# Kernel optimization log

Hardware: AMD Instinct MI355X
Metric: run time of the kernel (lower is better)

Reference implementation:

```python
import jax, jax.numpy as jnp
import numpy as np

MAX_RADIUS = 0.9
TEMP = 0.1

def _to_poincare(x, W, b):
    # Linear + Tanh, then rescale into Poincare ball of radius 0.9
    h = jnp.tanh(x @ W.T + b)
    norm = jnp.clip(jnp.linalg.norm(h, axis=-1, keepdims=True), 1e-8, None)
    scale = jnp.where(norm > MAX_RADIUS, MAX_RADIUS / norm, jnp.ones_like(norm))
    return h * scale

def setup_inputs() -> dict:
    key = jax.random.key(0)
    kq, kw, kb, km, ko = jax.random.split(key, 5)
    B, N, D = 2048, 100000, 128
    return {
        "query": jax.random.normal(kq, (B, D), dtype=jnp.float32),
        "W": jax.random.normal(kw, (D, D), dtype=jnp.float32) * (1.0 / np.sqrt(D)),
        "b": jax.random.normal(kb, (D,), dtype=jnp.float32) * 0.01,
        "mem_emb": jax.random.normal(km, (N, D), dtype=jnp.float32),
        "mem_out": jax.random.normal(ko, (N, D), dtype=jnp.float32),
        "k": 16,
    }

def reference(query, W, b, mem_emb, mem_out, k):
    q = _to_poincare(query, W, b)          # [B, D]
    m = _to_poincare(mem_emb, W, b)        # [N, D]
    # Euclidean cdist via the GEMM form: ||q||^2 + ||m||^2 - 2 q.m
    q2 = jnp.sum(q * q, axis=-1, keepdims=True)           # [B, 1]
    m2 = jnp.sum(m * m, axis=-1)                          # [N]
    d2 = q2 + m2[None, :] - 2.0 * (q @ m.T)               # [B, N]
    dists = jnp.sqrt(jnp.maximum(d2, 1e-12))
    # k smallest distances
    neg_top, top_idx = jax.lax.top_k(-dists, k)           # [B, k]
    top_dists = -neg_top
    weights = jax.nn.softmax(-top_dists / TEMP, axis=-1)  # [B, k]
    outcomes = mem_out[top_idx]                           # [B, k, D]
    return weights, outcomes
```

## Files before the change

### kernel.cpp

```cpp
#include <hip/hip_runtime.h>
#include <hip/hip_bf16.h>
#include <math.h>

#define DIM 128
#define QB 64
#define MB 64
#define NSPLIT 32
#define KSEL 16
#define KOWN 4
#define RESCORE 32
#define IDXMASK 0x1FFFu
#define KEYMASK 0xFFFFE000u

using bf16x8 = __attribute__((ext_vector_type(8))) short;
using f32x4  = __attribute__((ext_vector_type(4))) float;

__device__ inline unsigned short f2bf(float f) {
  __hip_bfloat16 h = __float2bfloat16(f);
  return __builtin_bit_cast(unsigned short, h);
}

__device__ inline f32x4 mfma16(bf16x8 a, bf16x8 b, f32x4 c) {
  return __builtin_amdgcn_mfma_f32_16x16x32_bf16(a, b, c, 0, 0, 0);
}

__device__ inline void gload_lds16(const void* g, void* l) {
  __builtin_amdgcn_global_load_lds(
      (const __attribute__((address_space(1))) void*)g,
      (__attribute__((address_space(3))) void*)l, 16, 0, 0);
}

__global__ __launch_bounds__(512) void poincare2_k(
    const float* __restrict__ Xm, int Rm,
    const float* __restrict__ Xq, int Rq,
    const float* __restrict__ W, const float* __restrict__ bias,
    float* __restrict__ Pm, float* __restrict__ Pm2,
    unsigned short* __restrict__ Pmbf,
    float* __restrict__ Pq, float* __restrict__ Pq2, int nbm)
{
  __shared__ float Wl[DIM * DIM];
  __shared__ float nrm[128 * 17];
  __shared__ float norm2l[128];

  const int t  = threadIdx.x;
  const int cg = t & 15;
  const int rg = t >> 4;

  const bool ismem = (int)blockIdx.x < nbm;
  const float* X = ismem ? Xm : Xq;
  const int    R = ismem ? Rm : Rq;
  float*       P  = ismem ? Pm  : Pq;
  float*       P2 = ismem ? Pm2 : Pq2;
  unsigned short* Pbf = ismem ? Pmbf : nullptr;
  const int rbase = (ismem ? blockIdx.x : (blockIdx.x - nbm)) * 128;

  for (int i = t; i < DIM * 32; i += 512) {
    const int j = i >> 5, c = i & 31;
    const float4 v = *(const float4*)&W[j * DIM + c * 4];
    *(float4*)&Wl[j * DIM + ((c ^ ((j >> 3) & 7)) << 2)] = v;
  }
  float bj[8];
  #pragma unroll
  for (int u = 0; u < 8; ++u) bj[u] = bias[cg * 8 + u];

  const float* xr[4];
  #pragma unroll
  for (int v = 0; v < 4; ++v) {
    int row = rbase + rg + 32 * v;
    if (row > R - 1) row = R - 1;
    xr[v] = X + (size_t)row * DIM;
  }
  __syncthreads();

  float acc[4][8];
  #pragma unroll
  for (int v = 0; v < 4; ++v)
    #pragma unroll
    for (int u = 0; u < 8; ++u) acc[v][u] = bj[u];

  #pragma unroll 2
  for (int k4 = 0; k4 < 32; ++k4) {
    float4 xv[4], wv[8];
    #pragma unroll
    for (int v = 0; v < 4; ++v) xv[v] = *(const float4*)&xr[v][k4 * 4];
    #pragma unroll
    for (int u = 0; u < 8; ++u) {
      const int j = cg * 8 + u;
      wv[u] = *(const float4*)&Wl[j * DIM + ((k4 ^ ((j >> 3) & 7)) << 2)];
    }
    #pragma unroll
    for (int v = 0; v < 4; ++v)
      #pragma unroll
      for (int u = 0; u < 8; ++u) {
        acc[v][u] = fmaf(xv[v].x, wv[u].x, acc[v][u]);
        acc[v][u] = fmaf(xv[v].y, wv[u].y, acc[v][u]);
        acc[v][u] = fmaf(xv[v].z, wv[u].z, acc[v][u]);
        acc[v][u] = fmaf(xv[v].w, wv[u].w, acc[v][u]);
      }
  }

  #pragma unroll
  for (int v = 0; v < 4; ++v) {
    float pn = 0.f;
    #pragma unroll
    for (int u = 0; u < 8; ++u) {
      const float th = tanhf(acc[v][u]);
      acc[v][u] = th;
      pn = fmaf(th, th, pn);
    }
    nrm[(rg + 32 * v) * 17 + cg] = pn;
  }
  __syncthreads();
  if (t < 128) {
    float s = 0.f;
    #pragma unroll
    for (int c2 = 0; c2 < 16; ++c2) s += nrm[t * 17 + c2];
    norm2l[t] = s;
    if (rbase + t < R) {
      const float nm = sqrtf(s);
      const float sc = (nm > 0.9f) ? (0.9f / nm) : 1.0f;
      P2[rbase + t] = s * sc * sc;
    }
  }
  __syncthreads();

  #pragma unroll
  for (int v = 0; v < 4; ++v) {
    const int r = rg + 32 * v;
    const int row = rbase + r;
    if (row < R) {
      const float n2 = norm2l[r];
      const float nm = sqrtf(n2);
      const float sc = (nm > 0.9f) ? (0.9f / nm) : 1.0f;
      float o[8];
      #pragma unroll
      for (int u = 0; u < 8; ++u) o[u] = acc[v][u] * sc;
      *(float4*)&P[(size_t)row * DIM + cg * 8]     = make_float4(o[0], o[1], o[2], o[3]);
      *(float4*)&P[(size_t)row * DIM + cg * 8 + 4] = make_float4(o[4], o[5], o[6], o[7]);
      if (Pbf) {
        uint4 pb;
        pb.x = (unsigned)f2bf(o[0]) | ((unsigned)f2bf(o[1]) << 16);
        pb.y = (unsigned)f2bf(o[2]) | ((unsigned)f2bf(o[3]) << 16);
        pb.z = (unsigned)f2bf(o[4]) | ((unsigned)f2bf(o[5]) << 16);
        pb.w = (unsigned)f2bf(o[6]) | ((unsigned)f2bf(o[7]) << 16);
        *(uint4*)&Pmbf[(size_t)row * DIM + ((cg ^ (row & 7)) << 3)] = pb;
      }
    }
  }
}

template<bool USEBF>
__global__ __launch_bounds__(512, 8) void score_topk_k(
    const float* __restrict__ Pq,
    const float* __restrict__ Pm, const float* __restrict__ Pm2,
    const unsigned short* __restrict__ Pmbf,
    int N, int splitlen, unsigned* __restrict__ splitTop)
{
  __shared__ __align__(16) unsigned short Ml0[MB * DIM];
  __shared__ __align__(16) unsigned short Ml1[MB * DIM];
  __shared__ float m20[MB], m21[MB];

  const int t = threadIdx.x;
  const int lane = t & 63;
  const int w = t >> 6, wr = w >> 1, wc = w & 1;
  const int split = blockIdx.x;
  const int qbase = blockIdx.y * QB;
  const int mlo = split * splitlen;
  const int mhi = min(mlo + splitlen, N);

  bf16x8 qf[4];
  {
    const int qrow = qbase + wr * 16 + (lane & 15);
    #pragma unroll
    for (int ks = 0; ks < 4; ++ks) {
      const float* src = &Pq[(size_t)qrow * DIM + ks * 32 + (lane >> 4) * 8];
      float4 lo = *(const float4*)src;
      float4 hi = *(const float4*)(src + 4);
      bf16x8 v;
      v[0] = (short)f2bf(lo.x); v[1] = (short)f2bf(lo.y);
      v[2] = (short)f2bf(lo.z); v[3] = (short)f2bf(lo.w);
      v[4] = (short)f2bf(hi.x); v[5] = (short)f2bf(hi.y);
      v[6] = (short)f2bf(hi.z); v[7] = (short)f2bf(hi.w);
      qf[ks] = v;
    }
  }

  const size_t soff0 = (size_t)(w * 8 + (lane >> 4)) * DIM + ((lane & 15) << 3);
  const size_t soff1 = soff0 + 4 * DIM;
  unsigned short* const d00 = &Ml0[(w * 8) * DIM];
  unsigned short* const d01 = &Ml0[(w * 8 + 4) * DIM];
  unsigned short* const d10 = &Ml1[(w * 8) * DIM];
  unsigned short* const d11 = &Ml1[(w * 8 + 4) * DIM];

  auto stage = [&](int mbase, unsigned short* dA, unsigned short* dB,
                   unsigned short* lds) {
    if constexpr (USEBF) {
      const unsigned short* b = Pmbf + (size_t)mbase * DIM;
      gload_lds16(b + soff0, dA);
      gload_lds16(b + soff1, dB);
    } else {
      const int fr = t >> 3, fe = t & 7;
      const float* src = Pm + (size_t)(mbase + fr) * DIM + fe * 16;
      float4 a0 = *(const float4*)(src + 0);
      float4 a1 = *(const float4*)(src + 4);
      float4 a2 = *(const float4*)(src + 8);
      float4 a3 = *(const float4*)(src + 12);
      uint4 o0, o1;
      o0.x = (unsigned)f2bf(a0.x) | ((unsigned)f2bf(a0.y) << 16);
      o0.y = (unsigned)f2bf(a0.z) | ((unsigned)f2bf(a0.w) << 16);
      o0.z = (unsigned)f2bf(a1.x) | ((unsigned)f2bf(a1.y) << 16);
      o0.w = (unsigned)f2bf(a1.z) | ((unsigned)f2bf(a1.w) << 16);
      o1.x = (unsigned)f2bf(a2.x) | ((unsigned)f2bf(a2.y) << 16);
      o1.y = (unsigned)f2bf(a2.z) | ((unsigned)f2bf(a2.w) << 16);
      o1.z = (unsigned)f2bf(a3.x) | ((unsigned)f2bf(a3.y) << 16);
      o1.w = (unsigned)f2bf(a3.z) | ((unsigned)f2bf(a3.w) << 16);
      char* base = (char*)lds + fr * 256;
      *(uint4*)(base + (((2 * fe)     ^ (fr & 7)) << 4)) = o0;
      *(uint4*)(base + (((2 * fe + 1) ^ (fr & 7)) << 4)) = o1;
    }
  };

  const int ntiles = (mhi - mlo + MB - 1) / MB;
  const int mcol = wc * 32 + (lane & 15);

  stage(mlo, d00, d01, Ml0);
  if (t < MB) {
    const int gr = mlo + t;
    m20[t] = (gr < mhi) ? (Pm2[gr] + 2.0f) : __int_as_float(0x7f800000);
  }
  __syncthreads();

  unsigned keys[4][KOWN];
  #pragma unroll
  for (int r = 0; r < 4; ++r)
    #pragma unroll
    for (int i = 0; i < KOWN; ++i) keys[r][i] = 0xFFFFFFFFu;

  auto body = [&](int tile, const unsigned short* ldsCur,
                  unsigned short* dA, unsigned short* dB, unsigned short* ldsNxt,
                  const float* m2cur, float* m2nxt) {
    const int mbase = mlo + tile * MB;
    const bool more = (tile + 1 < ntiles);
    if (more) {
      stage(mbase + MB, dA, dB, ldsNxt);
      if (t < MB) {
        const int gr = mbase + MB + t;
        m2nxt[t] = (gr < mhi) ? (Pm2[gr] + 2.0f) : __int_as_float(0x7f800000);
      }
    }

    const float m2a = m2cur[mcol];
    const float m2b = m2cur[mcol + 16];

    f32x4 acc0 = (f32x4){0.f, 0.f, 0.f, 0.f};
    f32x4 acc1 = (f32x4){0.f, 0.f, 0.f, 0.f};

    const int rowA = mcol;
    const int rowB = mcol + 16;
    __builtin_amdgcn_s_setprio(1);
    #pragma unroll
    for (int ks = 0; ks < 4; ++ks) {
      const int kb = ks * 64 + (lane >> 4) * 16;
      bf16x8 bfrA = *(const bf16x8*)((const char*)ldsCur + rowA * 256 +
                                     (kb ^ ((rowA & 7) << 4)));
      bf16x8 bfrB = *(const bf16x8*)((const char*)ldsCur + rowB * 256 +
                                     (kb ^ ((rowB & 7) << 4)));
      acc0 = mfma16(qf[ks], bfrA, acc0);
      acc1 = mfma16(qf[ks], bfrB, acc1);
    }
    __builtin_amdgcn_s_setprio(0);

    const unsigned idx0 = (unsigned)(tile * MB + mcol);
    #pragma unroll
    for (int r = 0; r < 4; ++r) {
      {
        const float d2 = fmaf(-2.0f, acc0[r], m2a);
        unsigned c = (__float_as_uint(d2) & KEYMASK) | idx0;
        #pragma unroll
        for (int i = 0; i < KOWN; ++i) {
          const unsigned lo = c < keys[r][i] ? c : keys[r][i];
          c = c < keys[r][i] ? keys[r][i] : c;
          keys[r][i] = lo;
        }
      }
      {
        const float d2 = fmaf(-2.0f, acc1[r], m2b);
        unsigned c = (__float_as_uint(d2) & KEYMASK) | (idx0 + 16);
        #pragma unroll
        for (int i = 0; i < KOWN; ++i) {
          const unsigned lo = c < keys[r][i] ? c : keys[r][i];
          c = c < keys[r][i] ? keys[r][i] : c;
          keys[r][i] = lo;
        }
      }
    }
    __syncthreads();
  };

  int tile = 0;
  while (true) {
    body(tile, Ml0, d10, d11, Ml1, m20, m21); if (++tile == ntiles) break;
    body(tile, Ml1, d00, d01, Ml0, m21, m20); if (++tile == ntiles) break;
  }

  #pragma unroll
  for (int r = 0; r < 4; ++r) {
    unsigned k0 = keys[r][0], k1 = keys[r][1];
    unsigned k2 = keys[r][2], k3 = keys[r][3];
    unsigned out = 0xFFFFFFFFu;
    for (int round = 0; round < 8; ++round) {
      unsigned g = k0, o;
      o = __shfl_xor(g, 1, 16); g = o < g ? o : g;
      o = __shfl_xor(g, 2, 16); g = o < g ? o : g;
      o = __shfl_xor(g, 4, 16); g = o < g ? o : g;
      o = __shfl_xor(g, 8, 16); g = o < g ? o : g;
      const bool mine = (k0 == g);
      k0 = mine ? k1 : k0;
      k1 = mine ? k2 : k1;
      k2 = mine ? k3 : k2;
      k3 = mine ? 0xFFFFFFFFu : k3;
      if ((lane & 15) == round) out = g;
    }
    const int q = qbase + wr * 16 + (lane >> 4) * 4 + r;
    if ((lane & 15) < 8)
      splitTop[(((size_t)q * NSPLIT + split) * 2 + wc) * 8 + (lane & 15)] = out;
  }
}

__global__ __launch_bounds__(256) void finalize_k(
    const unsigned* __restrict__ splitTop,
    const float* __restrict__ Pq, const float* __restrict__ Pq2,
    const float* __restrict__ Pm, const float* __restrict__ Pm2,
    const float* __restrict__ memOut, int N, int splitlen,
    float* __restrict__ outW, float* __restrict__ outO)
{
  const int q = blockIdx.x;
  const int t = threadIdx.x;
  __shared__ unsigned selKey[RESCORE];
  __shared__ int      selSrc[RESCORE];
  __shared__ unsigned long long keyx[RESCORE];
  __shared__ unsigned long long selB[KSEL];
  __shared__ float el[KSEL];

  if (t < 64) {
    const unsigned* gp = splitTop + (size_t)q * (NSPLIT * 2 * 8) + t * 8;
    unsigned a[8];
    #pragma unroll
    for (int i = 0; i < 8; ++i) a[i] = gp[i];
    for (int r = 0; r < RESCORE; ++r) {
      unsigned g = a[0], o;
      #pragma unroll
      for (int st = 1; st < 64; st <<= 1) { o = __shfl_xor(g, st); g = o < g ? o : g; }
      unsigned long long mask = __ballot(a[0] == g);
      const int fl = __ffsll((unsigned long long)mask) - 1;
      if (t == fl) {
        selKey[r] = g;
        selSrc[r] = t;
        #pragma unroll
        for (int i = 0; i < 7; ++i) a[i] = a[i + 1];
        a[7] = 0xFFFFFFFFu;
      }
    }
  }
  __syncthreads();

  {
    const int g = t >> 3, e = t & 7;
    const int gidx = (selSrc[g] >> 1) * splitlen + (int)(selKey[g] & IDXMASK);
    const float4* qr = (const float4*)&Pq[(size_t)q * DIM];
    const float4* mr = (const float4*)&Pm[(size_t)gidx * DIM];
    float s = 0.f;
    #pragma unroll
    for (int u = 0; u < 4; ++u) {
      float4 a = qr[e * 4 + u], b = mr[e * 4 + u];
      s = fmaf(a.x, b.x, s); s = fmaf(a.y, b.y, s);
      s = fmaf(a.z, b.z, s); s = fmaf(a.w, b.w, s);
    }
    s += __shfl_xor(s, 1, 8);
    s += __shfl_xor(s, 2, 8);
    s += __shfl_xor(s, 4, 8);
    if (e == 0) {
      float d2 = (Pq2[q] + Pm2[gidx]) - 2.0f * s;
      float dist = sqrtf(fmaxf(d2, 1e-12f));
      keyx[g] = (((unsigned long long)__float_as_uint(dist)) << 32) | (unsigned)gidx;
    }
  }
  __syncthreads();

  if (t < 64) {
    unsigned long long kk = (t < RESCORE) ? keyx[t] : ~0ull;
    for (int r = 0; r < KSEL; ++r) {
      unsigned long long g = kk;
      #pragma unroll
      for (int o = 1; o < 64; o <<= 1) {
        unsigned long long s = __shfl_xor(g, o);
        g = (s < g) ? s : g;
      }
      if (kk == g) kk = ~0ull;
      if (t == 0) selB[r] = g;
    }
  }
  __syncthreads();

  if (t < KSEL) {
    const float d  = __uint_as_float((unsigned)(selB[t] >> 32));
    const float d0 = __uint_as_float((unsigned)(selB[0] >> 32));
    el[t] = expf(-(d / 0.1f) + (d0 / 0.1f));
  }
  __syncthreads();
  if (t < KSEL) {
    float sum = 0.f;
    #pragma unroll
    for (int i = 0; i < KSEL; ++i) sum += el[i];
    outW[(size_t)q * KSEL + t] = el[t] / sum;
  }

  for (int f4 = t; f4 < KSEL * 32; f4 += 256) {
    int r = f4 >> 5, c4 = f4 & 31;
    int idx = (int)(selB[r] & 0xffffffffu);
    *(float4*)&outO[((size_t)q * KSEL + r) * DIM + c4 * 4] =
        *(const float4*)&memOut[(size_t)idx * DIM + c4 * 4];
  }
}

extern "C" void kernel_launch(void* const* d_in, const int* in_sizes, int n_in,
                              void* d_out, int out_size, void* d_ws, size_t ws_size,
                              hipStream_t stream)
{
  const float* query   = (const float*)d_in[0];
  const float* W       = (const float*)d_in[1];
  const float* bias    = (const float*)d_in[2];
  const float* mem_emb = (const float*)d_in[3];
  const float* mem_out = (const float*)d_in[4];
  const int B = in_sizes[0] / DIM;
  const int N = in_sizes[3] / DIM;
  const int N_pad = ((N + MB + 15) / 16) * 16;

  const int splitlen = ((N + NSPLIT * MB - 1) / (NSPLIT * MB)) * MB;

  float* ws  = (float*)d_ws;
  float* Pm  = ws;
  float* Pm2 = Pm + (size_t)N_pad * DIM;
  float* Pq  = Pm2 + N_pad;
  float* Pq2 = Pq + (size_t)B * DIM;
  unsigned* splitTop = (unsigned*)(Pq2 + B);
  unsigned short* Pmbf = (unsigned short*)(splitTop + (size_t)B * NSPLIT * 2 * 8);
  const size_t need_bf = (size_t)((char*)(Pmbf + (size_t)N_pad * DIM) - (char*)d_ws);
  const bool usebf = ws_size >= need_bf;

  float* outW = (float*)d_out;
  float* outO = outW + (size_t)B * KSEL;

  const int nbm = (N + 127) / 128;
  const int nbq = (B + 127) / 128;
  poincare2_k<<<dim3(nbm + nbq), dim3(512), 0, stream>>>(
      mem_emb, N, query, B, W, bias, Pm, Pm2, usebf ? Pmbf : nullptr, Pq, Pq2, nbm);

  dim3 grid2(NSPLIT, B / QB);
  if (usebf)
    score_topk_k<true><<<grid2, dim3(512), 0, stream>>>(Pq, Pm, Pm2, Pmbf, N,
                                                        splitlen, splitTop);
  else
    score_topk_k<false><<<grid2, dim3(512), 0, stream>>>(Pq, Pm, Pm2, nullptr, N,
                                                         splitlen, splitTop);

  finalize_k<<<dim3(B), dim3(256), 0, stream>>>(splitTop, Pq, Pq2, Pm, Pm2,
                                                mem_out, N, splitlen, outW, outO);
}
```

Measured before the change: 222.7 us.

## Fold distance offset into MFMA accumulator init and make finalize one query per wave

The query fragments are negated and the per-row m2 term is pre-scaled to 0.5*m2+1, so the MFMA accumulator starts at that bias and the score key comes straight from the accumulator without a separate fma. Compare-select pairs become explicit unsigned min/max builtins. The finalize kernel now handles four queries per block, one per wavefront, and drops all block-wide barriers in favour of per-wave shared arrays. This trades some rescaling of the key value, which keeps the same ordering, for fewer VALU ops in the hot scoring loop and less sync overhead in finalize.

```diff
diff --git a/kernel.cpp b/kernel.cpp
--- a/kernel.cpp
+++ b/kernel.cpp
@@ -18,6 +18,16 @@
 __device__ inline unsigned short f2bf(float f) {
   __hip_bfloat16 h = __float2bfloat16(f);
   return __builtin_bit_cast(unsigned short, h);
+}
+__device__ inline unsigned uminu(unsigned a, unsigned b) {
+  return __builtin_elementwise_min(a, b);
+}
+__device__ inline unsigned umaxu(unsigned a, unsigned b) {
+  return __builtin_elementwise_max(a, b);
+}
+__device__ inline unsigned long long umin64(unsigned long long a,
+                                            unsigned long long b) {
+  return __builtin_elementwise_min(a, b);
 }
 
 __device__ inline f32x4 mfma16(bf16x8 a, bf16x8 b, f32x4 c) {
@@ -177,10 +187,10 @@
       float4 lo = *(const float4*)src;
       float4 hi = *(const float4*)(src + 4);
       bf16x8 v;
-      v[0] = (short)f2bf(lo.x); v[1] = (short)f2bf(lo.y);
-      v[2] = (short)f2bf(lo.z); v[3] = (short)f2bf(lo.w);
-      v[4] = (short)f2bf(hi.x); v[5] = (short)f2bf(hi.y);
-      v[6] = (short)f2bf(hi.z); v[7] = (short)f2bf(hi.w);
+      v[0] = (short)f2bf(-lo.x); v[1] = (short)f2bf(-lo.y);
+      v[2] = (short)f2bf(-lo.z); v[3] = (short)f2bf(-lo.w);
+      v[4] = (short)f2bf(-hi.x); v[5] = (short)f2bf(-hi.y);
+      v[6] = (short)f2bf(-hi.z); v[7] = (short)f2bf(-hi.w);
       qf[ks] = v;
     }
   }
@@ -226,7 +236,8 @@
   stage(mlo, d00, d01, Ml0);
   if (t < MB) {
     const int gr = mlo + t;
-    m20[t] = (gr < mhi) ? (Pm2[gr] + 2.0f) : __int_as_float(0x7f800000);
+    m20[t] = (gr < mhi) ? fmaf(0.5f, Pm2[gr], 1.0f)
+                        : __int_as_float(0x7f800000);
   }
   __syncthreads();
 
@@ -245,15 +256,16 @@
       stage(mbase + MB, dA, dB, ldsNxt);
       if (t < MB) {
         const int gr = mbase + MB + t;
-        m2nxt[t] = (gr < mhi) ? (Pm2[gr] + 2.0f) : __int_as_float(0x7f800000);
-      }
-    }
-
-    const float m2a = m2cur[mcol];
-    const float m2b = m2cur[mcol + 16];
-
-    f32x4 acc0 = (f32x4){0.f, 0.f, 0.f, 0.f};
-    f32x4 acc1 = (f32x4){0.f, 0.f, 0.f, 0.f};
+        m2nxt[t] = (gr < mhi) ? fmaf(0.5f, Pm2[gr], 1.0f)
+                              : __int_as_float(0x7f800000);
+      }
+    }
+
+    const float ca = m2cur[mcol];
+    const float cb = m2cur[mcol + 16];
+
+    f32x4 acc0 = (f32x4){ca, ca, ca, ca};
+    f32x4 acc1 = (f32x4){cb, cb, cb, cb};
 
     const int rowA = mcol;
     const int rowB = mcol + 16;
@@ -274,22 +286,20 @@
     #pragma unroll
     for (int r = 0; r < 4; ++r) {
       {
-        const float d2 = fmaf(-2.0f, acc0[r], m2a);
-        unsigned c = (__float_as_uint(d2) & KEYMASK) | idx0;
+        unsigned c = (__float_as_uint(acc0[r]) & KEYMASK) | idx0;
         #pragma unroll
         for (int i = 0; i < KOWN; ++i) {
-          const unsigned lo = c < keys[r][i] ? c : keys[r][i];
-          c = c < keys[r][i] ? keys[r][i] : c;
+          const unsigned lo = uminu(c, keys[r][i]);
+          c = umaxu(c, keys[r][i]);
           keys[r][i] = lo;
         }
       }
       {
-        const float d2 = fmaf(-2.0f, acc1[r], m2b);
-        unsigned c = (__float_as_uint(d2) & KEYMASK) | (idx0 + 16);
+        unsigned c = (__float_as_uint(acc1[r]) & KEYMASK) | (idx0 + 16);
         #pragma unroll
         for (int i = 0; i < KOWN; ++i) {
-          const unsigned lo = c < keys[r][i] ? c : keys[r][i];
-          c = c < keys[r][i] ? keys[r][i] : c;
+          const unsigned lo = uminu(c, keys[r][i]);
+          c = umaxu(c, keys[r][i]);
           keys[r][i] = lo;
         }
       }
@@ -309,11 +319,11 @@
     unsigned k2 = keys[r][2], k3 = keys[r][3];
     unsigned out = 0xFFFFFFFFu;
     for (int round = 0; round < 8; ++round) {
-      unsigned g = k0, o;
-      o = __shfl_xor(g, 1, 16); g = o < g ? o : g;
-      o = __shfl_xor(g, 2, 16); g = o < g ? o : g;
-      o = __shfl_xor(g, 4, 16); g = o < g ? o : g;
-      o = __shfl_xor(g, 8, 16); g = o < g ? o : g;
+      unsigned g = k0;
+      g = uminu(g, __shfl_xor(g, 1, 16));
+      g = uminu(g, __shfl_xor(g, 2, 16));
+      g = uminu(g, __shfl_xor(g, 4, 16));
+      g = uminu(g, __shfl_xor(g, 8, 16));
       const bool mine = (k0 == g);
       k0 = mine ? k1 : k0;
       k1 = mine ? k2 : k1;
@@ -334,39 +344,47 @@
     const float* __restrict__ memOut, int N, int splitlen,
     float* __restrict__ outW, float* __restrict__ outO)
 {
-  const int q = blockIdx.x;
-  const int t = threadIdx.x;
-  __shared__ unsigned selKey[RESCORE];
-  __shared__ int      selSrc[RESCORE];
-  __shared__ unsigned long long keyx[RESCORE];
-  __shared__ unsigned long long selB[KSEL];
-  __shared__ float el[KSEL];
-
-  if (t < 64) {
-    const unsigned* gp = splitTop + (size_t)q * (NSPLIT * 2 * 8) + t * 8;
+  const int wv   = threadIdx.x >> 6;
+  const int lane = threadIdx.x & 63;
+  const int q = blockIdx.x * 4 + wv;
+
+  __shared__ unsigned      sKey[4][RESCORE];
+  __shared__ unsigned char sSrc[4][RESCORE];
+  __shared__ unsigned long long sKeyx[4][RESCORE];
+  __shared__ unsigned long long sSel[4][KSEL];
+  __shared__ float sEl[4][KSEL];
+
+  {
+    const unsigned* gp = splitTop + (size_t)q * (NSPLIT * 2 * 8) + lane * 8;
     unsigned a[8];
-    #pragma unroll
-    for (int i = 0; i < 8; ++i) a[i] = gp[i];
+    uint4 lo = *(const uint4*)gp;
+    uint4 hi = *(const uint4*)(gp + 4);
+    a[0] = lo.x; a[1] = lo.y; a[2] = lo.z; a[3] = lo.w;
+    a[4] = hi.x; a[5] = hi.y; a[6] = hi.z; a[7] = hi.w;
     for (int r = 0; r < RESCORE; ++r) {
-      unsigned g = a[0], o;
-      #pragma unroll
-      for (int st = 1; st < 64; st <<= 1) { o = __shfl_xor(g, st); g = o < g ? o : g; }
+      unsigned g = a[0];
+      g = uminu(g, __shfl_xor(g, 1));
+      g = uminu(g, __shfl_xor(g, 2));
+      g = uminu(g, __shfl_xor(g, 4));
+      g = uminu(g, __shfl_xor(g, 8));
+      g = uminu(g, __shfl_xor(g, 16));
+      g = uminu(g, __shfl_xor(g, 32));
       unsigned long long mask = __ballot(a[0] == g);
       const int fl = __ffsll((unsigned long long)mask) - 1;
-      if (t == fl) {
-        selKey[r] = g;
-        selSrc[r] = t;
+      if (lane == fl) {
         #pragma unroll
         for (int i = 0; i < 7; ++i) a[i] = a[i + 1];
         a[7] = 0xFFFFFFFFu;
       }
-    }
-  }
-  __syncthreads();
-
-  {
-    const int g = t >> 3, e = t & 7;
-    const int gidx = (selSrc[g] >> 1) * splitlen + (int)(selKey[g] & IDXMASK);
+      if (lane == 0) { sKey[wv][r] = g; sSrc[wv][r] = (unsigned char)fl; }
+    }
+  }
+
+  #pragma unroll
+  for (int p = 0; p < 4; ++p) {
+    const int g8 = p * 8 + (lane >> 3), e = lane & 7;
+    const int src = sSrc[wv][g8];
+    const int gidx = (src >> 1) * splitlen + (int)(sKey[wv][g8] & IDXMASK);
     const float4* qr = (const float4*)&Pq[(size_t)q * DIM];
     const float4* mr = (const float4*)&Pm[(size_t)gidx * DIM];
     float s = 0.f;
@@ -382,42 +400,43 @@
     if (e == 0) {
       float d2 = (Pq2[q] + Pm2[gidx]) - 2.0f * s;
       float dist = sqrtf(fmaxf(d2, 1e-12f));
-      keyx[g] = (((unsigned long long)__float_as_uint(dist)) << 32) | (unsigned)gidx;
-    }
-  }
-  __syncthreads();
-
-  if (t < 64) {
-    unsigned long long kk = (t < RESCORE) ? keyx[t] : ~0ull;
+      sKeyx[wv][g8] =
+          (((unsigned long long)__float_as_uint(dist)) << 32) | (unsigned)gidx;
+    }
+  }
+
+  {
+    unsigned long long kk = (lane < RESCORE) ? sKeyx[wv][lane] : ~0ull;
     for (int r = 0; r < KSEL; ++r) {
       unsigned long long g = kk;
-      #pragma unroll
-      for (int o = 1; o < 64; o <<= 1) {
-        unsigned long long s = __shfl_xor(g, o);
-        g = (s < g) ? s : g;
-      }
+      g = umin64(g, __shfl_xor(g, 1));
+      g = umin64(g, __shfl_xor(g, 2));
+      g = umin64(g, __shfl_xor(g, 4));
+      g = umin64(g, __shfl_xor(g, 8));
+      g = umin64(g, __shfl_xor(g, 16));
+      g = umin64(g, __shfl_xor(g, 32));
       if (kk == g) kk = ~0ull;
-      if (t == 0) selB[r] = g;
-    }
-  }
-  __syncthreads();
-
-  if (t < KSEL) {
-    const float d  = __uint_as_float((unsigned)(selB[t] >> 32));
-    const float d0 = __uint_as_float((unsigned)(selB[0] >> 32));
-    el[t] = expf(-(d / 0.1f) + (d0 / 0.1f));
-  }
-  __syncthreads();
-  if (t < KSEL) {
+      if (lane == 0) sSel[wv][r] = g;
+    }
+  }
+
+  if (lane < KSEL) {
+    const float d  = __uint_as_float((unsigned)(sSel[wv][lane] >> 32));
+    const float d0 = __uint_as_float((unsigned)(sSel[wv][0] >> 32));
+    sEl[wv][lane] = expf((d0 - d) * 10.0f);
+  }
+  if (lane < KSEL) {
     float sum = 0.f;
     #pragma unroll
-    for (int i = 0; i < KSEL; ++i) sum += el[i];
-    outW[(size_t)q * KSEL + t] = el[t] / sum;
-  }
-
-  for (int f4 = t; f4 < KSEL * 32; f4 += 256) {
-    int r = f4 >> 5, c4 = f4 & 31;
-    int idx = (int)(selB[r] & 0xffffffffu);
+    for (int i = 0; i < KSEL; ++i) sum += sEl[wv][i];
+    outW[(size_t)q * KSEL + lane] = sEl[wv][lane] / sum;
+  }
+
+  #pragma unroll
+  for (int i = 0; i < 8; ++i) {
+    const int f4 = lane + i * 64;
+    const int r = f4 >> 5, c4 = f4 & 31;
+    const int idx = (int)(sSel[wv][r] & 0xffffffffu);
     *(float4*)&outO[((size_t)q * KSEL + r) * DIM + c4 * 4] =
         *(const float4*)&memOut[(size_t)idx * DIM + c4 * 4];
   }
@@ -464,6 +483,7 @@
     score_topk_k<false><<<grid2, dim3(512), 0, stream>>>(Pq, Pm, Pm2, nullptr, N,
                                                          splitlen, splitTop);
 
-  finalize_k<<<dim3(B), dim3(256), 0, stream>>>(splitTop, Pq, Pq2, Pm, Pm2,
-                                                mem_out, N, splitlen, outW, outO);
-}
+  finalize_k<<<dim3(B / 4), dim3(256), 0, stream>>>(splitTop, Pq, Pq2, Pm, Pm2,
+                                                    mem_out, N, splitlen,
+                                                    outW, outO);
+}
```

New measurement: 219.4 us. No clear change (-1.5%).
